# Optimization experiments

Hardware: AMD Instinct MI355X
Metric: run time of the kernel (lower is better)

## Reference

```python
import jax, jax.numpy as jnp
import numpy as np

OUT_H, OUT_W = 7, 7
SPATIAL_SCALE = 1.0  # aligned=True (align_corners=True interpolate), per init_kwargs


def setup_inputs() -> dict:
    key = jax.random.key(0)
    kf, kb, kx, ky, kw, kh = jax.random.split(key, 6)
    B, C, H, W = 4, 256, 200, 200
    N = 512
    features = jax.random.normal(kf, (B, C, H, W), dtype=jnp.float32)
    batch_idx = jax.random.randint(kb, (N,), 0, B, dtype=jnp.int32)
    # integer boxes with x2>x1, y2>y1, strictly inside the map
    x1 = jax.random.randint(kx, (N,), 0, W - 64, dtype=jnp.int32)
    y1 = jax.random.randint(ky, (N,), 0, H - 64, dtype=jnp.int32)
    bw = jax.random.randint(kw, (N,), 8, 64, dtype=jnp.int32)
    bh = jax.random.randint(kh, (N,), 8, 64, dtype=jnp.int32)
    x2 = jnp.minimum(x1 + bw, W - 1)
    y2 = jnp.minimum(y1 + bh, H - 1)
    rois = jnp.stack([batch_idx, x1, y1, x2, y2], axis=1)  # [N, 5] int32
    return {"features": features, "rois": rois}


def reference(features, rois):
    # features: [B, C, H, W]; rois: [N, 5] int32 (batch, x1, y1, x2, y2)
    # Faithful to: crop features[b, :, y1:y2+1, x1:x2+1] then
    # F.interpolate(size=(7,7), mode='bilinear', align_corners=True).
    N = rois.shape[0]
    H, W = features.shape[2], features.shape[3]
    b = rois[:, 0]
    coords = rois[:, 1:5].astype(jnp.float32) * SPATIAL_SCALE
    x1, y1, x2, y2 = coords[:, 0], coords[:, 1], coords[:, 2], coords[:, 3]

    # align_corners=True source coords inside the crop, offset into the full map
    jy = jnp.arange(OUT_H, dtype=jnp.float32)
    jx = jnp.arange(OUT_W, dtype=jnp.float32)
    sy = y1[:, None] + jy[None, :] * (y2 - y1)[:, None] / (OUT_H - 1)  # [N, OH]
    sx = x1[:, None] + jx[None, :] * (x2 - x1)[:, None] / (OUT_W - 1)  # [N, OW]

    y0f = jnp.floor(sy); x0f = jnp.floor(sx)
    wy = sy - y0f                                  # [N, OH]
    wx = sx - x0f                                  # [N, OW]
    y0 = jnp.clip(y0f.astype(jnp.int32), 0, H - 1)
    y1i = jnp.clip(y0 + 1, 0, H - 1)
    x0 = jnp.clip(x0f.astype(jnp.int32), 0, W - 1)
    x1i = jnp.clip(x0 + 1, 0, W - 1)

    bb = b[:, None, None]                          # [N,1,1]

    def gather(yi, xi):
        # advanced indexing -> [N, OH, OW, C]
        return features[bb, :, yi[:, :, None], xi[:, None, :]]

    v00 = gather(y0, x0)
    v01 = gather(y0, x1i)
    v10 = gather(y1i, x0)
    v11 = gather(y1i, x1i)

    wyb = wy[:, :, None, None]                     # [N, OH, 1, 1]
    wxb = wx[:, None, :, None]                     # [N, 1, OW, 1]
    out = (v00 * (1 - wyb) * (1 - wxb) + v01 * (1 - wyb) * wxb
           + v10 * wyb * (1 - wxb) + v11 * wyb * wxb)  # [N, OH, OW, C]
    return jnp.transpose(out, (0, 3, 1, 2))        # [N, C, OH, OW]
```

## Files before the change

### kernel.cpp

```cpp
#include <hip/hip_runtime.h>
#include <hip/hip_bf16.h>
#include <string.h>

#define OUT_H 7
#define OUT_W 7
#define FEAT_H 200
#define FEAT_W 200
#define HW_ALL (FEAT_H * FEAT_W)
#define THW 160
#define TLS 161

__device__ inline unsigned pack2_bf16(float a, float b) {
    __hip_bfloat16 ha = __float2bfloat16(a);
    __hip_bfloat16 hb = __float2bfloat16(b);
    unsigned short ua, ub;
    memcpy(&ua, &ha, 2);
    memcpy(&ub, &hb, 2);
    return (unsigned)ua | ((unsigned)ub << 16);
}

__global__ __launch_bounds__(256) void nchw_to_blocked_v4(
    const float* __restrict__ feat,
    uint2*       __restrict__ featT,
    int HW)
{
    __shared__ float tile[64 * TLS];
    int hw0 = blockIdx.x * THW;
    int cg  = blockIdx.y;
    int b   = blockIdx.z;
    const float* src = feat + ((size_t)b * 256 + cg * 64) * HW + hw0;
    int t = threadIdx.x;

#pragma unroll
    for (int i = 0; i < 10; ++i) {
        int flat = i * 256 + t;
        int c = flat / 40;
        int q = flat % 40;
        float4 v = *(const float4*)(src + (size_t)c * HW + q * 4);
        float* d = &tile[c * TLS + q * 4];
        d[0] = v.x; d[1] = v.y; d[2] = v.z; d[3] = v.w;
    }
    __syncthreads();

    uint2* dst = featT + ((size_t)(b * 4 + cg) * HW + hw0) * 16;
#pragma unroll
    for (int i = 0; i < 10; ++i) {
        int o  = i * 256 + t;
        int hw = o >> 4;
        int cq = o & 15;
        float a0 = tile[(cq * 4 + 0) * TLS + hw];
        float a1 = tile[(cq * 4 + 1) * TLS + hw];
        float a2 = tile[(cq * 4 + 2) * TLS + hw];
        float a3 = tile[(cq * 4 + 3) * TLS + hw];
        uint2 u;
        u.x = pack2_bf16(a0, a1);
        u.y = pack2_bf16(a2, a3);
        dst[o] = u;
    }
}

__global__ __launch_bounds__(256) void roialign_blocked_v4(
    const uint2* __restrict__ featT,
    const int*   __restrict__ rois,
    float*       __restrict__ out)
{
    __shared__ float acc[64 * OUT_H * OUT_W];
    const int H = FEAT_H, W = FEAT_W;
    int n  = blockIdx.x >> 2;
    int cg = blockIdx.x & 3;
    const int* r = rois + n * 5;
    int   b   = r[0];
    float x1f = (float)r[1];
    float y1f = (float)r[2];
    float dx  = (float)r[3] - x1f;
    float dy  = (float)r[4] - y1f;

    int t  = threadIdx.x;
    int cq = t & 15;
    int pg = t >> 4;
    const uint2* fb = featT + ((size_t)(b * 4 + cg) * HW_ALL) * 16 + cq;

#define BFLO(u) __uint_as_float((u) << 16)
#define BFHI(u) __uint_as_float((u) & 0xffff0000u)

#pragma unroll
    for (int pi = 0; pi < 4; ++pi) {
        int p = (pi << 4) + pg;
        if (p < 49) {
            int jy = p / 7, jx = p % 7;
            float sy = y1f + ((float)jy * dy) / 6.0f;
            float sx = x1f + ((float)jx * dx) / 6.0f;
            float y0fl = floorf(sy), x0fl = floorf(sx);
            float wy = sy - y0fl,    wx = sx - x0fl;
            int y0  = min(max((int)y0fl, 0), H - 1);
            int y1i = min(y0 + 1, H - 1);
            int x0  = min(max((int)x0fl, 0), W - 1);
            int x1i = min(x0 + 1, W - 1);
            float omwy = 1.0f - wy, omwx = 1.0f - wx;
            float w00 = omwy * omwx, w01 = omwy * wx;
            float w10 = wy * omwx,   w11 = wy * wx;

            uint2 u00 = fb[(size_t)(y0  * W + x0 ) * 16];
            uint2 u01 = fb[(size_t)(y0  * W + x1i) * 16];
            uint2 u10 = fb[(size_t)(y1i * W + x0 ) * 16];
            uint2 u11 = fb[(size_t)(y1i * W + x1i) * 16];

            float r0 = BFLO(u00.x)*w00 + BFLO(u01.x)*w01 + BFLO(u10.x)*w10 + BFLO(u11.x)*w11;
            float r1 = BFHI(u00.x)*w00 + BFHI(u01.x)*w01 + BFHI(u10.x)*w10 + BFHI(u11.x)*w11;
            float r2 = BFLO(u00.y)*w00 + BFLO(u01.y)*w01 + BFLO(u10.y)*w10 + BFLO(u11.y)*w11;
            float r3 = BFHI(u00.y)*w00 + BFHI(u01.y)*w01 + BFHI(u10.y)*w10 + BFHI(u11.y)*w11;

            int c0 = cq << 2;
            acc[(c0 + 0) * 49 + p] = r0;
            acc[(c0 + 1) * 49 + p] = r1;
            acc[(c0 + 2) * 49 + p] = r2;
            acc[(c0 + 3) * 49 + p] = r3;
        }
    }
    __syncthreads();

    float* ob = out + ((size_t)n * 256 + cg * 64) * (OUT_H * OUT_W);
    const int total = 64 * OUT_H * OUT_W;
    for (int k = t; k < total; k += 256)
        ob[k] = acc[k];
}

__global__ __launch_bounds__(256) void roialign_direct(
    const float* __restrict__ feat, const int* __restrict__ rois,
    float* __restrict__ out, int C, int H, int W, int total)
{
    int idx = blockIdx.x * blockDim.x + threadIdx.x;
    if (idx >= total) return;
    int jx = idx % OUT_W;
    int t  = idx / OUT_W;
    int jy = t % OUT_H;
    t /= OUT_H;
    int c = t % C;
    int n = t / C;
    const int* r = rois + n * 5;
    int b = r[0];
    float x1 = (float)r[1], y1 = (float)r[2];
    float x2 = (float)r[3], y2 = (float)r[4];
    float sy = y1 + ((float)jy * (y2 - y1)) / (float)(OUT_H - 1);
    float sx = x1 + ((float)jx * (x2 - x1)) / (float)(OUT_W - 1);
    float y0f = floorf(sy), x0f = floorf(sx);
    float wy = sy - y0f, wx = sx - x0f;
    int y0  = min(max((int)y0f, 0), H - 1);
    int y1i = min(y0 + 1, H - 1);
    int x0  = min(max((int)x0f, 0), W - 1);
    int x1i = min(x0 + 1, W - 1);
    const float* fp = feat + ((size_t)b * C + c) * (size_t)(H * W);
    float v00 = fp[y0  * W + x0 ];
    float v01 = fp[y0  * W + x1i];
    float v10 = fp[y1i * W + x0 ];
    float v11 = fp[y1i * W + x1i];
    float omwy = 1.0f - wy, omwx = 1.0f - wx;
    out[idx] = v00 * omwy * omwx + v01 * omwy * wx
             + v10 * wy   * omwx + v11 * wy   * wx;
}

extern "C" void kernel_launch(void* const* d_in, const int* in_sizes, int n_in,
                              void* d_out, int out_size, void* d_ws, size_t ws_size,
                              hipStream_t stream)
{
    const float* feat = (const float*)d_in[0];
    const int*   rois = (const int*)d_in[1];
    float*       out  = (float*)d_out;

    int N  = in_sizes[1] / 5;
    int C  = out_size / (N * OUT_H * OUT_W);
    int B  = in_sizes[0] / (C * HW_ALL);

    size_t need = (size_t)B * HW_ALL * 256 * sizeof(__hip_bfloat16);
    if (C == 256 && in_sizes[0] == B * 256 * HW_ALL && ws_size >= need) {
        uint2* featT = (uint2*)d_ws;
        dim3 tgrid(HW_ALL / THW, 4, B);
        nchw_to_blocked_v4<<<tgrid, 256, 0, stream>>>(feat, featT, HW_ALL);
        roialign_blocked_v4<<<N * 4, 256, 0, stream>>>(featT, rois, out);
    } else {
        int total = out_size;
        roialign_direct<<<(total + 255) / 256, 256, 0, stream>>>(
            feat, rois, out, C, FEAT_H, FEAT_W, total);
    }
}
```

Measured before the change: 257.1 us.

## Rewrite NCHW-to-blocked bf16 transpose as persistent per-wave tiles

Replaces the block-wide 64x160 shared-memory transpose with a persistent grid of 2048 blocks in which each wave independently transposes 64 channels x 16 pixels through its own padded LDS slice. Waves sync with wave barriers instead of __syncthreads and use less LDS per block, aiming for more occupancy and better overlap in this bandwidth-bound layout conversion. In exchange, each lane reads a 64-byte strip from a different channel row, so global reads are less contiguous per instruction, and the grid-stride loop adds index arithmetic.

```diff
diff --git a/kernel.cpp b/kernel.cpp
--- a/kernel.cpp
+++ b/kernel.cpp
@@ -7,8 +7,7 @@
 #define FEAT_H 200
 #define FEAT_W 200
 #define HW_ALL (FEAT_H * FEAT_W)
-#define THW 160
-#define TLS 161
+#define TPW 17
 
 __device__ inline unsigned pack2_bf16(float a, float b) {
     __hip_bfloat16 ha = __float2bfloat16(a);
@@ -19,43 +18,53 @@
     return (unsigned)ua | ((unsigned)ub << 16);
 }
 
-__global__ __launch_bounds__(256) void nchw_to_blocked_v4(
+__global__ __launch_bounds__(256) void nchw_to_blocked_v5(
     const float* __restrict__ feat,
     uint2*       __restrict__ featT,
-    int HW)
+    int nunits)
 {
-    __shared__ float tile[64 * TLS];
-    int hw0 = blockIdx.x * THW;
-    int cg  = blockIdx.y;
-    int b   = blockIdx.z;
-    const float* src = feat + ((size_t)b * 256 + cg * 64) * HW + hw0;
-    int t = threadIdx.x;
+    __shared__ float lds[4][64 * TPW];
+    int wid  = threadIdx.x >> 6;
+    int lane = threadIdx.x & 63;
+    float* Ws = lds[wid];
 
+    int gwave  = blockIdx.x * 4 + wid;
+    int nwaves = gridDim.x * 4;
+    const int UPH = HW_ALL / 16;
+
+    for (int u = gwave; u < nunits; u += nwaves) {
+        int pc  = u / UPH;
+        int hw0 = (u - pc * UPH) * 16;
+
+        const float4* src = (const float4*)(feat + ((size_t)pc * 64 + lane) * HW_ALL + hw0);
+        float4 v0 = src[0];
+        float4 v1 = src[1];
+        float4 v2 = src[2];
+        float4 v3 = src[3];
+
+        float* row = &Ws[lane * TPW];
+        row[0]=v0.x;  row[1]=v0.y;  row[2]=v0.z;  row[3]=v0.w;
+        row[4]=v1.x;  row[5]=v1.y;  row[6]=v1.z;  row[7]=v1.w;
+        row[8]=v2.x;  row[9]=v2.y;  row[10]=v2.z; row[11]=v2.w;
+        row[12]=v3.x; row[13]=v3.y; row[14]=v3.z; row[15]=v3.w;
+
+        __builtin_amdgcn_wave_barrier();
+
+        uint2* dst = featT + ((size_t)pc * HW_ALL + hw0) * 16;
+        int q = lane & 15;
 #pragma unroll
-    for (int i = 0; i < 10; ++i) {
-        int flat = i * 256 + t;
-        int c = flat / 40;
-        int q = flat % 40;
-        float4 v = *(const float4*)(src + (size_t)c * HW + q * 4);
-        float* d = &tile[c * TLS + q * 4];
-        d[0] = v.x; d[1] = v.y; d[2] = v.z; d[3] = v.w;
-    }
-    __syncthreads();
+        for (int s = 0; s < 4; ++s) {
+            int flat = s * 64 + lane;
+            int hw_loc = s * 4 + (lane >> 4);
+            uint2 o;
+            o.x = pack2_bf16(Ws[(4*q + 0) * TPW + hw_loc],
+                             Ws[(4*q + 1) * TPW + hw_loc]);
+            o.y = pack2_bf16(Ws[(4*q + 2) * TPW + hw_loc],
+                             Ws[(4*q + 3) * TPW + hw_loc]);
+            dst[flat] = o;
+        }
 
-    uint2* dst = featT + ((size_t)(b * 4 + cg) * HW + hw0) * 16;
-#pragma unroll
-    for (int i = 0; i < 10; ++i) {
-        int o  = i * 256 + t;
-        int hw = o >> 4;
-        int cq = o & 15;
-        float a0 = tile[(cq * 4 + 0) * TLS + hw];
-        float a1 = tile[(cq * 4 + 1) * TLS + hw];
-        float a2 = tile[(cq * 4 + 2) * TLS + hw];
-        float a3 = tile[(cq * 4 + 3) * TLS + hw];
-        uint2 u;
-        u.x = pack2_bf16(a0, a1);
-        u.y = pack2_bf16(a2, a3);
-        dst[o] = u;
+        __builtin_amdgcn_wave_barrier();
     }
 }
 
@@ -174,8 +183,8 @@
     size_t need = (size_t)B * HW_ALL * 256 * sizeof(__hip_bfloat16);
     if (C == 256 && in_sizes[0] == B * 256 * HW_ALL && ws_size >= need) {
         uint2* featT = (uint2*)d_ws;
-        dim3 tgrid(HW_ALL / THW, 4, B);
-        nchw_to_blocked_v4<<<tgrid, 256, 0, stream>>>(feat, featT, HW_ALL);
+        int nunits = B * 4 * (HW_ALL / 16);
+        nchw_to_blocked_v5<<<2048, 256, 0, stream>>>(feat, featT, nunits);
         roialign_blocked_v4<<<N * 4, 256, 0, stream>>>(featT, rois, out);
     } else {
         int total = out_size;
```

Result: slower. 263.8 us (+2.6%).
